# Kernel tuning notes

Measured on AMD Instinct MI355X. Metric: run time of the kernel, lower is better.

Reference implementation:

```python
import jax, jax.numpy as jnp
import numpy as np


def setup_inputs() -> dict:
    key = jax.random.key(0)
    k1, k2, k3, k4 = jax.random.split(key, 4)
    B, C_in, C_out, H, W = 8, 256, 256, 160, 160
    mask = jax.random.randint(k1, (B, 1, H, W), 0, 2, dtype=jnp.int32)  # binary hard mask
    ori = jax.random.normal(k2, (B, C_in, H, W), dtype=jnp.float32)
    weight = jax.random.normal(k3, (C_out, C_in, 3, 3), dtype=jnp.float32) * 0.02
    bias = jax.random.normal(k4, (C_out,), dtype=jnp.float32) * 0.02
    return {"mask": mask, "ori": ori, "weight": weight, "bias": bias}


def reference(mask, ori, weight, bias):
    # apply_mask: broadcast binary [B,1,H,W] mask over channels, zero masked regions
    x = ori * mask.astype(ori.dtype)
    # dense 3x3 conv, stride 1, padding 1 (SAME) -> output [B, C_out, H, W]
    out = jax.lax.conv_general_dilated(
        x, weight,
        window_strides=(1, 1),
        padding='SAME',
        dimension_numbers=('NCHW', 'OIHW', 'NCHW'),
    )
    return out + bias[None, :, None, None]
```

## Files before the change

kernel.cpp:

```cpp
#include <hip/hip_runtime.h>

typedef __attribute__((ext_vector_type(8))) short short8;
typedef __attribute__((ext_vector_type(4))) float f32x4;

#define B_    8
#define CI    256
#define CO    256
#define Hh    160
#define Ww    160
#define HP    162
#define WP    162
#define HWp   (Hh * Ww)
#define XPAD_ELEMS (B_ * HP * WP * CI)
#define W3_ELEMS   (9 * CI * CO)
#define NT    36
#define BSLOT (160 * 64)

#define NBORD 644
#define NPW   2304
#define NPX   (B_ * Hh * 4 * 3)

__device__ __forceinline__ unsigned short f2bf(float f) {
  unsigned int u = __float_as_uint(f);
  u += 0x7FFFu + ((u >> 16) & 1u);
  return (unsigned short)(u >> 16);
}

__global__ void prep_all(const float* __restrict__ ori, const int* __restrict__ mask,
                         const float* __restrict__ w,
                         unsigned short* __restrict__ xp, unsigned short* __restrict__ w3) {
  __shared__ float tile[64][65];
  const int bid = blockIdx.x;
  const int t = threadIdx.x;

  if (bid < NBORD) {
    int g = bid * 256 + t;
    int pos = g >> 5;
    int c = (g & 31) << 3;
    int n = pos / 644;
    int p = pos - n * 644;
    int y, x;
    if (p < 324) { y = (p < 162) ? 0 : 161; x = (p < 162) ? p : p - 162; }
    else { int q = p - 324; y = 1 + (q >> 1); x = (q & 1) ? 161 : 0; }
    unsigned short* d = xp + (((size_t)(n * 162 + y)) * 162 + x) * 256 + c;
    *(uint4*)d = (uint4){0u, 0u, 0u, 0u};
    return;
  }
  if (bid < NBORD + NPW) {
    int i = (bid - NBORD) * 256 + t;
    int e = i & 7, l = (i >> 3) & 63, g = i >> 9;
    int mi = g & 1, wm = (g >> 1) & 3, kk = (g >> 3) & 1;
    int qm = (g >> 4) & 1, cic = (g >> 5) & 3, shift = g >> 7;
    int co = qm * 128 + wm * 32 + mi * 16 + (l & 15);
    int ci = cic * 64 + kk * 32 + (l >> 4) * 8 + e;
    w3[i] = f2bf(w[(co * 256 + ci) * 9 + shift]);
    return;
  }

  int bid2 = bid - (NBORD + NPW);
  int wt = bid2 % 3;
  int t1 = bid2 / 3;
  int cit = t1 & 3;
  int t2 = t1 >> 2;
  int h = t2 % Hh;
  int n = t2 / Hh;

  int wl = t & 63;
  int ww = wt * 64 + wl;
  bool valid = (ww < Ww);
  float m = 0.f;
  if (valid) m = (float)mask[(n * Hh + h) * Ww + ww];
  const float* src = ori + (((size_t)(n * CI + cit * 64) * Hh + h) * Ww + ww);
  int r0 = t >> 6;
#pragma unroll
  for (int k = 0; k < 16; ++k) {
    int ci_l = r0 * 16 + k;
    float v = 0.f;
    if (valid) v = src[(size_t)ci_l * HWp] * m;
    tile[ci_l][wl] = v;
  }
  __syncthreads();

  int wl2 = t >> 2;
  int wo = wt * 64 + wl2;
  if (wo < Ww) {
    int cseg = (t & 3) * 16;
    union { unsigned short u[8]; uint4 v; } p0, p1;
#pragma unroll
    for (int j = 0; j < 8; ++j) p0.u[j] = f2bf(tile[cseg + j][wl2]);
#pragma unroll
    for (int j = 0; j < 8; ++j) p1.u[j] = f2bf(tile[cseg + 8 + j][wl2]);
    unsigned short* dst = xp + ((size_t)((n * HP + h + 1) * WP) + (wo + 1)) * CI + cit * 64 + cseg;
    *(uint4*)dst = p0.v;
    *(uint4*)(dst + 8) = p1.v;
  }
}

__device__ __forceinline__ void gload16(const unsigned short* g, unsigned short* l) {
  __builtin_amdgcn_global_load_lds((const __attribute__((address_space(1))) void*)g,
                                   (__attribute__((address_space(3))) void*)l, 16, 0, 0);
}

__global__ void __launch_bounds__(256, 2)
sconv_gemm(const unsigned short* __restrict__ xp, const unsigned short* __restrict__ w3,
           const float* __restrict__ bias, float* __restrict__ out) {
  __shared__ unsigned short Bs[3][BSLOT];

  const int bid = blockIdx.x;
  const int n = bid & 7;
  const int h = bid >> 3;

  const int t = threadIdx.x;
  const int l = t & 63;
  const int wv = t >> 6;

  const int lr = l >> 3;
  const int swz8 = ((l & 7) ^ lr) << 3;
  const int lc = l & 15, hi4 = l >> 4, lx7 = l & 7;
  const unsigned xrow = (unsigned)(n * HP + h);

  unsigned boff[5];
#pragma unroll
  for (int k = 0; k < 5; ++k)
    boff[k] = (unsigned)(k * 32 + wv * 8 + lr) * 256 + swz8;

  f32x4 acc[4][10];
#pragma unroll
  for (int j = 0; j < 4; ++j)
#pragma unroll
    for (int ni = 0; ni < 10; ++ni)
      acc[j][ni] = (f32x4){0.f, 0.f, 0.f, 0.f};

  short8 aK0[4], aK1[4], bb[5];

#define TPAR(ts, cic, sh, kh, kw)                                             \
  const int cic = ((ts) * 57) >> 9;                                           \
  const int sh = (ts) - cic * 9;                                              \
  const int kh = (sh * 11) >> 5;                                              \
  const int kw = sh - kh * 3;

  auto STG = [&](int ts, unsigned short* slot, int k) {
    TPAR(ts, cic, sh, kh, kw)
    (void)sh;
    const unsigned short* src = xp + ((size_t)(xrow + kh) * WP + kw) * 256 + (cic << 6) + boff[k];
    gload16(src, slot + (k * 32 + wv * 8) * 64);
  };

  auto AGH = [&](int ts, int kk, short8* dst) {
    TPAR(ts, cic, sh, kh, kw)
    (void)kh; (void)kw;
    const unsigned short* p = w3 +
        ((size_t)(sh * 128 + cic * 32 + (wv >> 1) * 16 + ((wv & 1) << 2) + kk * 8) << 9) + (l << 3);
#pragma unroll
    for (int j = 0; j < 4; ++j)
      dst[j] = *(const short8*)(p + (j << 9));
  };

#define BBR(slot, kk, nb) do {                                                \
  _Pragma("unroll")                                                           \
  for (int i = 0; i < 5; ++i)                                                 \
    bb[i] = *(const short8*)((slot) + (((nb) + i) * 16 + lc) * 64 +           \
                             (((((kk) << 2) + hi4) ^ lx7) << 3));             \
} while (0)

#define CL(AH, nb) do {                                                       \
  __builtin_amdgcn_s_setprio(1);                                              \
  _Pragma("unroll")                                                           \
  for (int j = 0; j < 4; ++j)                                                 \
    _Pragma("unroll")                                                         \
    for (int i = 0; i < 5; ++i)                                               \
      acc[j][(nb) + i] = __builtin_amdgcn_mfma_f32_16x16x32_bf16(             \
          AH[j], bb[i], acc[j][(nb) + i], 0, 0, 0);                           \
  __builtin_amdgcn_s_setprio(0);                                              \
} while (0)

#define PH(slot, kk, AH, nb, ISSUES, ENDW) do {                               \
  ISSUES                                                                      \
  BBR(slot, kk, nb);                                                          \
  __builtin_amdgcn_s_barrier();                                               \
  CL(AH, nb);                                                                 \
  ENDW                                                                        \
  __builtin_amdgcn_s_barrier();                                               \
} while (0)

#define TILE(tt, sc, sn) do {                                                 \
  PH(sc, 0, aK0, 0, { STG((tt) + 2, sn, 0); STG((tt) + 2, sn, 1); }, {});     \
  PH(sc, 0, aK0, 5, { STG((tt) + 2, sn, 2); }, {});                           \
  PH(sc, 1, aK1, 0, { AGH((tt) + 1, 0, aK0); STG((tt) + 2, sn, 3); }, {});    \
  PH(sc, 1, aK1, 5, { STG((tt) + 2, sn, 4); },                                \
     { AGH((tt) + 1, 1, aK1);                                                 \
       asm volatile("s_waitcnt vmcnt(13)" ::: "memory"); });                  \
} while (0)

  unsigned short* const s0 = &Bs[0][0];
  unsigned short* const s1 = &Bs[1][0];
  unsigned short* const s2 = &Bs[2][0];

  for (int k = 0; k < 5; ++k) STG(0, s0, k);
  for (int k = 0; k < 5; ++k) STG(1, s1, k);
  AGH(0, 0, aK0);
  AGH(0, 1, aK1);
  asm volatile("s_waitcnt vmcnt(13)" ::: "memory");
  __builtin_amdgcn_s_barrier();

  for (int t3 = 0; t3 < 33; t3 += 3) {
    TILE(t3 + 0, s0, s2);
    TILE(t3 + 1, s1, s0);
    TILE(t3 + 2, s2, s1);
  }
  TILE(33, s0, s2);
  PH(s1, 0, aK0, 0, {}, {});
  PH(s1, 0, aK0, 5, {}, {});
  PH(s1, 1, aK1, 0, { AGH(35, 0, aK0); }, {});
  PH(s1, 1, aK1, 5, {},
     { AGH(35, 1, aK1);
       asm volatile("s_waitcnt vmcnt(8)" ::: "memory"); });
  PH(s2, 0, aK0, 0, {}, {});
  PH(s2, 0, aK0, 5, {}, {});
  PH(s2, 1, aK1, 0, {}, {});
  {
    BBR(s2, 1, 5);
    CL(aK1, 5);
  }

#pragma unroll
  for (int j = 0; j < 4; ++j) {
    int cobase = wv * 64 + j * 16 + hi4 * 4;
    const float4 bv = *(const float4*)(bias + cobase);
    float* op = out + (((size_t)n * CO + cobase) * Hh + h) * Ww;
#pragma unroll
    for (int ni = 0; ni < 10; ++ni) {
      int w = ni * 16 + lc;
      f32x4 v = acc[j][ni];
      op[w]                   = v[0] + bv.x;
      op[(size_t)HWp + w]     = v[1] + bv.y;
      op[(size_t)2 * HWp + w] = v[2] + bv.z;
      op[(size_t)3 * HWp + w] = v[3] + bv.w;
    }
  }
}

extern "C" void kernel_launch(void* const* d_in, const int* in_sizes, int n_in,
                              void* d_out, int out_size, void* d_ws, size_t ws_size,
                              hipStream_t stream) {
  const int* mask = (const int*)d_in[0];
  const float* ori = (const float*)d_in[1];
  const float* weight = (const float*)d_in[2];
  const float* bias = (const float*)d_in[3];
  float* out = (float*)d_out;

  unsigned short* xp = (unsigned short*)d_ws;
  unsigned short* w3 = xp + XPAD_ELEMS;

  prep_all<<<NBORD + NPW + NPX, 256, 0, stream>>>(ori, mask, weight, xp, w3);
  sconv_gemm<<<1280, 256, 0, stream>>>(xp, w3, bias, out);
}
```

Baseline: 309.1 us.

## Split output channels across two blocks and use 2x2 wave tiling

Each block now handles half of the output channels (128) for one output row rather than all 256, which doubles the grid to 2560 blocks. The four waves are arranged 2x2 over channels and width, so each wave holds 4x5 accumulators instead of 4x10, and each tile runs two phases instead of four. The aim is to cut register pressure and raise occupancy and load balance. The cost is that every activation row tile is staged into LDS twice, once per channel half, and there are relatively more barriers per MFMA.

```diff
diff --git a/kernel.cpp b/kernel.cpp
--- a/kernel.cpp
+++ b/kernel.cpp
@@ -108,11 +108,15 @@
 
   const int bid = blockIdx.x;
   const int n = bid & 7;
-  const int h = bid >> 3;
+  const int rest = bid >> 3;
+  const int cohalf = rest & 1;
+  const int h = rest >> 1;
 
   const int t = threadIdx.x;
   const int l = t & 63;
   const int wv = t >> 6;
+  const int wm = wv >> 1;
+  const int wn = wv & 1;
 
   const int lr = l >> 3;
   const int swz8 = ((l & 7) ^ lr) << 3;
@@ -124,11 +128,11 @@
   for (int k = 0; k < 5; ++k)
     boff[k] = (unsigned)(k * 32 + wv * 8 + lr) * 256 + swz8;
 
-  f32x4 acc[4][10];
+  f32x4 acc[4][5];
 #pragma unroll
   for (int j = 0; j < 4; ++j)
 #pragma unroll
-    for (int ni = 0; ni < 10; ++ni)
+    for (int ni = 0; ni < 5; ++ni)
       acc[j][ni] = (f32x4){0.f, 0.f, 0.f, 0.f};
 
   short8 aK0[4], aK1[4], bb[5];
@@ -150,44 +154,45 @@
     TPAR(ts, cic, sh, kh, kw)
     (void)kh; (void)kw;
     const unsigned short* p = w3 +
-        ((size_t)(sh * 128 + cic * 32 + (wv >> 1) * 16 + ((wv & 1) << 2) + kk * 8) << 9) + (l << 3);
+        ((size_t)(sh * 128 + cic * 32 + cohalf * 16 + kk * 8 + wm * 4) << 9) + (l << 3);
 #pragma unroll
     for (int j = 0; j < 4; ++j)
       dst[j] = *(const short8*)(p + (j << 9));
   };
 
-#define BBR(slot, kk, nb) do {                                                \
+#define BBR(slot, kk) do {                                                    \
   _Pragma("unroll")                                                           \
   for (int i = 0; i < 5; ++i)                                                 \
-    bb[i] = *(const short8*)((slot) + (((nb) + i) * 16 + lc) * 64 +           \
+    bb[i] = *(const short8*)((slot) + ((wn * 80 + i * 16 + lc) * 64) +        \
                              (((((kk) << 2) + hi4) ^ lx7) << 3));             \
 } while (0)
 
-#define CL(AH, nb) do {                                                       \
+#define CL(AH) do {                                                           \
   __builtin_amdgcn_s_setprio(1);                                              \
   _Pragma("unroll")                                                           \
   for (int j = 0; j < 4; ++j)                                                 \
     _Pragma("unroll")                                                         \
     for (int i = 0; i < 5; ++i)                                               \
-      acc[j][(nb) + i] = __builtin_amdgcn_mfma_f32_16x16x32_bf16(             \
-          AH[j], bb[i], acc[j][(nb) + i], 0, 0, 0);                           \
+      acc[j][i] = __builtin_amdgcn_mfma_f32_16x16x32_bf16(                    \
+          AH[j], bb[i], acc[j][i], 0, 0, 0);                                  \
   __builtin_amdgcn_s_setprio(0);                                              \
 } while (0)
 
-#define PH(slot, kk, AH, nb, ISSUES, ENDW) do {                               \
+#define PH(slot, kk, AH, ISSUES, ENDW) do {                                   \
   ISSUES                                                                      \
-  BBR(slot, kk, nb);                                                          \
+  BBR(slot, kk);                                                              \
   __builtin_amdgcn_s_barrier();                                               \
-  CL(AH, nb);                                                                 \
+  CL(AH);                                                                     \
   ENDW                                                                        \
   __builtin_amdgcn_s_barrier();                                               \
 } while (0)
 
 #define TILE(tt, sc, sn) do {                                                 \
-  PH(sc, 0, aK0, 0, { STG((tt) + 2, sn, 0); STG((tt) + 2, sn, 1); }, {});     \
-  PH(sc, 0, aK0, 5, { STG((tt) + 2, sn, 2); }, {});                           \
-  PH(sc, 1, aK1, 0, { AGH((tt) + 1, 0, aK0); STG((tt) + 2, sn, 3); }, {});    \
-  PH(sc, 1, aK1, 5, { STG((tt) + 2, sn, 4); },                                \
+  PH(sc, 0, aK0,                                                              \
+     { STG((tt) + 2, sn, 0); STG((tt) + 2, sn, 1); STG((tt) + 2, sn, 2); },   \
+     {});                                                                     \
+  PH(sc, 1, aK1,                                                              \
+     { AGH((tt) + 1, 0, aK0); STG((tt) + 2, sn, 3); STG((tt) + 2, sn, 4); },  \
      { AGH((tt) + 1, 1, aK1);                                                 \
        asm volatile("s_waitcnt vmcnt(13)" ::: "memory"); });                  \
 } while (0)
@@ -209,28 +214,24 @@
     TILE(t3 + 2, s2, s1);
   }
   TILE(33, s0, s2);
-  PH(s1, 0, aK0, 0, {}, {});
-  PH(s1, 0, aK0, 5, {}, {});
-  PH(s1, 1, aK1, 0, { AGH(35, 0, aK0); }, {});
-  PH(s1, 1, aK1, 5, {},
+  PH(s1, 0, aK0, {}, {});
+  PH(s1, 1, aK1, { AGH(35, 0, aK0); },
      { AGH(35, 1, aK1);
        asm volatile("s_waitcnt vmcnt(8)" ::: "memory"); });
-  PH(s2, 0, aK0, 0, {}, {});
-  PH(s2, 0, aK0, 5, {}, {});
-  PH(s2, 1, aK1, 0, {}, {});
+  PH(s2, 0, aK0, {}, {});
   {
-    BBR(s2, 1, 5);
-    CL(aK1, 5);
+    BBR(s2, 1);
+    CL(aK1);
   }
 
 #pragma unroll
   for (int j = 0; j < 4; ++j) {
-    int cobase = wv * 64 + j * 16 + hi4 * 4;
+    int cobase = cohalf * 128 + wm * 64 + j * 16 + hi4 * 4;
     const float4 bv = *(const float4*)(bias + cobase);
     float* op = out + (((size_t)n * CO + cobase) * Hh + h) * Ww;
 #pragma unroll
-    for (int ni = 0; ni < 10; ++ni) {
-      int w = ni * 16 + lc;
+    for (int ni = 0; ni < 5; ++ni) {
+      int w = wn * 80 + ni * 16 + lc;
       f32x4 v = acc[j][ni];
       op[w]                   = v[0] + bv.x;
       op[(size_t)HWp + w]     = v[1] + bv.y;
@@ -253,5 +254,5 @@
   unsigned short* w3 = xp + XPAD_ELEMS;
 
   prep_all<<<NBORD + NPW + NPX, 256, 0, stream>>>(ori, mask, weight, xp, w3);
-  sconv_gemm<<<1280, 256, 0, stream>>>(xp, w3, bias, out);
-}
+  sconv_gemm<<<2560, 256, 0, stream>>>(xp, w3, bias, out);
+}
```

After: 339.3 us. +9.8%, slower.
